# Optimization experiments

Hardware: AMD Instinct MI355X
Metric: run time of the kernel (lower is better)

## Reference

```python
import jax, jax.numpy as jnp
import numpy as np

B, S, F_IN, F_OUT, K = 4, 4096, 64, 64, 32


def setup_inputs() -> dict:
    key = jax.random.key(0)
    k1, k2, k3 = jax.random.split(key, 3)
    X = jax.random.normal(k1, (B, S, F_IN), dtype=jnp.float32)
    M = jax.random.normal(k2, (B, S, K), dtype=jnp.float32)
    # xavier_uniform for weight: bound = sqrt(6/(fan_in+fan_out))
    bound = float(np.sqrt(6.0 / (F_IN + F_OUT)))
    weight = jax.random.uniform(k3, (F_IN, F_OUT), dtype=jnp.float32,
                                minval=-bound, maxval=bound)
    bias = jnp.zeros((F_OUT,), dtype=jnp.float32)
    return {"X": X, "M": M, "weight": weight, "bias": bias}


def reference(X, M, weight, bias):
    # similarity = softmax(relu(M M^T), axis=-1)  -> [B, S, S]
    sim_raw = jnp.einsum('bsk,btk->bst', M, M)
    sim = jax.nn.softmax(jax.nn.relu(sim_raw), axis=-1)
    # X W  -> [B, S, F_OUT]
    Xw = jnp.einsum('bsf,fo->bso', X, weight)
    # mode='add': (I + A) Xw = Xw + A @ Xw  (identity matmul folded)
    Z = Xw + jnp.einsum('bst,bto->bso', sim, Xw)
    Z = Z + bias
    # dropout is identity at inference (eval mode)
    return Z
```

## Files before the change

### kernel.cpp

```cpp
#include <hip/hip_runtime.h>
#include <cstdint>

#define BATCH  4
#define SLEN   4096
#define FDIM   64
#define KDIM   32
#define KSPLIT 8
#define CHUNK  (SLEN / KSPLIT)

typedef __attribute__((ext_vector_type(8))) short bf16x8;
typedef __attribute__((ext_vector_type(4))) short bf16x4;
typedef __attribute__((ext_vector_type(4))) float f32x4;

static __device__ __forceinline__ short f2bf(float f) {
    union { float f; unsigned u; } v; v.f = f;
    unsigned r = v.u + 0x7fffu + ((v.u >> 16) & 1u);
    return (short)(r >> 16);
}
static __device__ __forceinline__ float bf2f(short s) {
    union { unsigned u; float f; } v;
    v.u = ((unsigned)(unsigned short)s) << 16;
    return v.f;
}
static __device__ __forceinline__ unsigned pack2bf(float a, float b) {
    union { float f; unsigned u; } x, y; x.f = a; y.f = b;
    unsigned ra = x.u + 0x7fffu + ((x.u >> 16) & 1u);
    unsigned rb = y.u + 0x7fffu + ((y.u >> 16) & 1u);
    return __builtin_amdgcn_perm(rb, ra, 0x07060302u);
}

__global__ __launch_bounds__(256) void prep(const float4* __restrict__ M4,
                                            ushort4* __restrict__ H4,
                                            ushort4* __restrict__ L4,
                                            const float* __restrict__ X,
                                            const float4* __restrict__ W4,
                                            float4* __restrict__ V4,
                                            short* __restrict__ Vt) {
    const int blk = blockIdx.y * gridDim.x + blockIdx.x;
#pragma unroll
    for (int r = 0; r < 2; ++r) {
        int i = (blk * 2 + r) * 256 + threadIdx.x;
        float4 m = M4[i];
        ushort4 h, l;
        h.x = (unsigned short)f2bf(m.x); l.x = (unsigned short)f2bf(m.x - bf2f((short)h.x));
        h.y = (unsigned short)f2bf(m.y); l.y = (unsigned short)f2bf(m.y - bf2f((short)h.y));
        h.z = (unsigned short)f2bf(m.z); l.z = (unsigned short)f2bf(m.z - bf2f((short)h.z));
        h.w = (unsigned short)f2bf(m.w); l.w = (unsigned short)f2bf(m.w - bf2f((short)h.w));
        H4[i] = h; L4[i] = l;
    }
    __shared__ float t[64][65];
    const int b  = blockIdx.y;
    const int s0 = blockIdx.x * 64;
    const int o4 = threadIdx.x & 15;
    const int rq = threadIdx.x >> 4;
#pragma unroll
    for (int half = 0; half < 4; ++half) {
        int r = half * 16 + rq;
        const float* __restrict__ xr = X + ((size_t)b * SLEN + s0 + r) * FDIM;
        float4 acc = make_float4(0.f, 0.f, 0.f, 0.f);
#pragma unroll
        for (int f = 0; f < FDIM; ++f) {
            float4 w = W4[f * 16 + o4];
            float  x = xr[f];
            acc.x = fmaf(x, w.x, acc.x);
            acc.y = fmaf(x, w.y, acc.y);
            acc.z = fmaf(x, w.z, acc.z);
            acc.w = fmaf(x, w.w, acc.w);
        }
        V4[((size_t)b * SLEN + s0 + r) * 16 + o4] = acc;
        t[r][o4 * 4 + 0] = acc.x;
        t[r][o4 * 4 + 1] = acc.y;
        t[r][o4 * 4 + 2] = acc.z;
        t[r][o4 * 4 + 3] = acc.w;
    }
    __syncthreads();
    const int c0 = threadIdx.x & 63;
    const int r0 = threadIdx.x >> 6;
#pragma unroll
    for (int i = 0; i < 16; ++i) {
        int f = r0 + i * 4;
        Vt[((size_t)b * FDIM + f) * SLEN + s0 + c0] = f2bf(t[c0][f]);
    }
}

__global__ __launch_bounds__(256, 3) void attn_mfma(const short* __restrict__ Mhi,
                                                    const short* __restrict__ Mlo,
                                                    const short* __restrict__ Vt,
                                                    float* __restrict__ accP,
                                                    float* __restrict__ lP) {
    const int bid  = blockIdx.x;
    const int slab = (bid & 7) + 8 * (bid >> 8);
    const int qblk = (bid >> 3) & 31;
    const int b    = slab >> 3;
    const int ks   = slab & 7;

    const int tid  = threadIdx.x;
    const int wave = tid >> 6;
    const int lane = tid & 63;
    const int col  = lane & 15;
    const int quad = lane >> 4;
    const int qbase = qblk * 128 + wave * 32;
    const int k0    = ks * CHUNK;

    const short* __restrict__ Mbh = Mhi + (size_t)b * SLEN * KDIM;
    const short* __restrict__ Mbl = Mlo + (size_t)b * SLEN * KDIM;
    const short* __restrict__ Vb  = Vt  + (size_t)b * FDIM * SLEN;

    __shared__ short khi[32 * 40];
    __shared__ short klo[32 * 40];
    __shared__ short vsh[64 * 40];

    bf16x8 Qh[2], Ql[2];
#pragma unroll
    for (int tq = 0; tq < 2; ++tq) {
        int qo = (qbase + tq * 16 + col) * KDIM + quad * 8;
        Qh[tq] = *(const bf16x8*)(Mbh + qo);
        Ql[tq] = *(const bf16x8*)(Mbl + qo);
    }

    f32x4 accf[2][4];
#pragma unroll
    for (int tq = 0; tq < 2; ++tq)
#pragma unroll
        for (int fg = 0; fg < 4; ++fg) accf[tq][fg] = (f32x4){0.f, 0.f, 0.f, 0.f};
    float lacc[2] = {0.f, 0.f};

    const int krow  = (tid & 127) >> 2;
    const int kpart = tid & 3;
    const int vrow  = tid >> 2;
    const short* __restrict__ Msrc = (tid < 128) ? Mbh : Mbl;
    short* __restrict__ kdst = (tid < 128) ? khi : klo;

#pragma unroll 1
    for (int kt = k0; kt < k0 + CHUNK; kt += 32) {
        bf16x8 kstg = *(const bf16x8*)(Msrc + (kt + krow) * KDIM + kpart * 8);
        bf16x8 vstg = *(const bf16x8*)(Vb + (size_t)vrow * SLEN + kt + kpart * 8);
        __syncthreads();
        *(bf16x8*)(kdst + krow * 40 + kpart * 8) = kstg;
        *(bf16x8*)(vsh + vrow * 40 + kpart * 8)  = vstg;
        __syncthreads();

        bf16x8 Kh0 = *(const bf16x8*)(khi + col * 40 + quad * 8);
        bf16x8 Kh1 = *(const bf16x8*)(khi + (16 + col) * 40 + quad * 8);
        bf16x8 Kl0 = *(const bf16x8*)(klo + col * 40 + quad * 8);
        bf16x8 Kl1 = *(const bf16x8*)(klo + (16 + col) * 40 + quad * 8);

        bf16x8 Vv[4];
#pragma unroll
        for (int fg = 0; fg < 4; ++fg) {
            const short* vp = vsh + (fg * 16 + col) * 40 + quad * 4;
            bf16x4 vlo = *(const bf16x4*)(vp);
            bf16x4 vhi = *(const bf16x4*)(vp + 16);
            Vv[fg] = __builtin_shufflevector(vlo, vhi, 0, 1, 2, 3, 4, 5, 6, 7);
        }

#pragma unroll
        for (int tq = 0; tq < 2; ++tq) {
            f32x4 z = (f32x4){0.f, 0.f, 0.f, 0.f};
            f32x4 c0 = __builtin_amdgcn_mfma_f32_16x16x32_bf16(Kh0, Ql[tq], z, 0, 0, 0);
            f32x4 c1 = __builtin_amdgcn_mfma_f32_16x16x32_bf16(Kh1, Ql[tq], z, 0, 0, 0);
            c0 = __builtin_amdgcn_mfma_f32_16x16x32_bf16(Kl0, Qh[tq], c0, 0, 0, 0);
            c1 = __builtin_amdgcn_mfma_f32_16x16x32_bf16(Kl1, Qh[tq], c1, 0, 0, 0);
            c0 = __builtin_amdgcn_mfma_f32_16x16x32_bf16(Kh0, Qh[tq], c0, 0, 0, 0);
            c1 = __builtin_amdgcn_mfma_f32_16x16x32_bf16(Kh1, Qh[tq], c1, 0, 0, 0);

            float e00 = __expf(fmaxf(c0[0], 0.f));
            float e01 = __expf(fmaxf(c0[1], 0.f));
            float e02 = __expf(fmaxf(c0[2], 0.f));
            float e03 = __expf(fmaxf(c0[3], 0.f));
            float e10 = __expf(fmaxf(c1[0], 0.f));
            float e11 = __expf(fmaxf(c1[1], 0.f));
            float e12 = __expf(fmaxf(c1[2], 0.f));
            float e13 = __expf(fmaxf(c1[3], 0.f));
            lacc[tq] += ((e00 + e01) + (e02 + e03)) + ((e10 + e11) + (e12 + e13));

            union { unsigned u[4]; bf16x8 v; } pa;
            pa.u[0] = pack2bf(e00, e01);
            pa.u[1] = pack2bf(e02, e03);
            pa.u[2] = pack2bf(e10, e11);
            pa.u[3] = pack2bf(e12, e13);

#pragma unroll
            for (int fg = 0; fg < 4; ++fg)
                accf[tq][fg] = __builtin_amdgcn_mfma_f32_16x16x32_bf16(
                    pa.v, Vv[fg], accf[tq][fg], 0, 0, 0);
        }
    }

#pragma unroll
    for (int tq = 0; tq < 2; ++tq) {
#pragma unroll
        for (int j = 0; j < 4; ++j) {
            int q = qbase + tq * 16 + quad * 4 + j;
            size_t base = ((size_t)b * SLEN + q) * KSPLIT + ks;
            float* __restrict__ op = accP + base * FDIM;
#pragma unroll
            for (int fg = 0; fg < 4; ++fg)
                op[fg * 16 + col] = accf[tq][fg][j];
        }
        float lv = lacc[tq];
        lv += __shfl_xor(lv, 16);
        lv += __shfl_xor(lv, 32);
        if (quad == 0) {
            int q = qbase + tq * 16 + col;
            lP[((size_t)b * SLEN + q) * KSPLIT + ks] = lv;
        }
    }
}

__global__ __launch_bounds__(256) void combine_kernel(const float4* __restrict__ V4,
                                                      const float4* __restrict__ accP4,
                                                      const float* __restrict__ lP,
                                                      const float4* __restrict__ bias4,
                                                      float4* __restrict__ out4) {
    int i  = blockIdx.x * 256 + threadIdx.x;
    int o4 = i & 15;
    int row = i >> 4;
    float nx = 0.f, ny = 0.f, nz = 0.f, nw = 0.f, den = 0.f;
#pragma unroll
    for (int k = 0; k < KSPLIT; ++k) {
        float4 a = accP4[((size_t)row * KSPLIT + k) * 16 + o4];
        nx += a.x; ny += a.y; nz += a.z; nw += a.w;
        den += lP[(size_t)row * KSPLIT + k];
    }
    float r = 1.f / den;
    float4 v = V4[i];
    float4 bb = bias4[o4];
    float4 o;
    o.x = v.x + nx * r + bb.x;
    o.y = v.y + ny * r + bb.y;
    o.z = v.z + nz * r + bb.z;
    o.w = v.w + nw * r + bb.w;
    out4[i] = o;
}

extern "C" void kernel_launch(void* const* d_in, const int* in_sizes, int n_in,
                              void* d_out, int out_size, void* d_ws, size_t ws_size,
                              hipStream_t stream) {
    const float* X    = (const float*)d_in[0];
    const float* M    = (const float*)d_in[1];
    const float* W    = (const float*)d_in[2];
    const float* bias = (const float*)d_in[3];
    float* out = (float*)d_out;

    const size_t vElems = (size_t)BATCH * SLEN * FDIM;
    const size_t mElems = (size_t)BATCH * SLEN * KDIM;
    const size_t rows   = (size_t)BATCH * SLEN;

    float* Vf   = (float*)d_ws;
    float* accP = Vf + vElems;
    float* lP   = accP + vElems * KSPLIT;
    short* Mhi  = (short*)(lP + rows * KSPLIT);
    short* Mlo  = Mhi + mElems;
    short* Vt   = Mlo + mElems;

    prep<<<dim3(SLEN / 64, BATCH), 256, 0, stream>>>(
        (const float4*)M, (ushort4*)Mhi, (ushort4*)Mlo,
        X, (const float4*)W, (float4*)Vf, Vt);

    attn_mfma<<<dim3((SLEN / 128) * BATCH * KSPLIT), 256, 0, stream>>>(
        Mhi, Mlo, Vt, accP, lP);

    combine_kernel<<<(int)(vElems / 1024), 256, 0, stream>>>(
        (const float4*)Vf, (const float4*)accP, lP, (const float4*)bias,
        (float4*)out);
}
```

Before: 120.7 us.

## Double-buffer LDS tiles in attention loop and switch to exp2 with prescaled M

The attention kernel now keeps two LDS buffers for the K and V tiles. It prefetches the next tile's global loads into registers while the current one is computed, which cuts the two barriers per iteration down to one and hides global load latency. M is prescaled by sqrt(log2 e) in prep, so the hardware exp2 replaces __expf without changing the math. It also raises wave priority around the MFMA section, gives prep more, smaller blocks with vectorized X loads, and vectorizes the denominator loads in combine. The cost is extra LDS use, which may limit occupancy, and a small rounding change from scaling before the bf16 split.

Measured after the change: 113.1 us. 6.4% less time.

```diff
diff --git a/kernel.cpp b/kernel.cpp
--- a/kernel.cpp
+++ b/kernel.cpp
@@ -7,10 +7,19 @@
 #define KDIM   32
 #define KSPLIT 8
 #define CHUNK  (SLEN / KSPLIT)
+#define NSTEP  (CHUNK / 32)
+
+#define MSCALE 1.2011224087864498f
 
 typedef __attribute__((ext_vector_type(8))) short bf16x8;
 typedef __attribute__((ext_vector_type(4))) short bf16x4;
 typedef __attribute__((ext_vector_type(4))) float f32x4;
+
+#if __has_builtin(__builtin_amdgcn_exp2f)
+#define EXP2(x) __builtin_amdgcn_exp2f(x)
+#else
+#define EXP2(x) exp2f(x)
+#endif
 
 static __device__ __forceinline__ short f2bf(float f) {
     union { float f; unsigned u; } v; v.f = f;
@@ -32,54 +41,55 @@
 __global__ __launch_bounds__(256) void prep(const float4* __restrict__ M4,
                                             ushort4* __restrict__ H4,
                                             ushort4* __restrict__ L4,
-                                            const float* __restrict__ X,
+                                            const float4* __restrict__ X4,
                                             const float4* __restrict__ W4,
                                             float4* __restrict__ V4,
                                             short* __restrict__ Vt) {
+    const int tid = threadIdx.x;
     const int blk = blockIdx.y * gridDim.x + blockIdx.x;
-#pragma unroll
-    for (int r = 0; r < 2; ++r) {
-        int i = (blk * 2 + r) * 256 + threadIdx.x;
+    if (blk < (BATCH * SLEN * KDIM) / (4 * 256)) {
+        int i = blk * 256 + tid;
         float4 m = M4[i];
+        float mx = m.x * MSCALE, my = m.y * MSCALE;
+        float mz = m.z * MSCALE, mw = m.w * MSCALE;
         ushort4 h, l;
-        h.x = (unsigned short)f2bf(m.x); l.x = (unsigned short)f2bf(m.x - bf2f((short)h.x));
-        h.y = (unsigned short)f2bf(m.y); l.y = (unsigned short)f2bf(m.y - bf2f((short)h.y));
-        h.z = (unsigned short)f2bf(m.z); l.z = (unsigned short)f2bf(m.z - bf2f((short)h.z));
-        h.w = (unsigned short)f2bf(m.w); l.w = (unsigned short)f2bf(m.w - bf2f((short)h.w));
+        h.x = (unsigned short)f2bf(mx); l.x = (unsigned short)f2bf(mx - bf2f((short)h.x));
+        h.y = (unsigned short)f2bf(my); l.y = (unsigned short)f2bf(my - bf2f((short)h.y));
+        h.z = (unsigned short)f2bf(mz); l.z = (unsigned short)f2bf(mz - bf2f((short)h.z));
+        h.w = (unsigned short)f2bf(mw); l.w = (unsigned short)f2bf(mw - bf2f((short)h.w));
         H4[i] = h; L4[i] = l;
     }
-    __shared__ float t[64][65];
+    __shared__ float t[16][68];
     const int b  = blockIdx.y;
-    const int s0 = blockIdx.x * 64;
-    const int o4 = threadIdx.x & 15;
-    const int rq = threadIdx.x >> 4;
-#pragma unroll
-    for (int half = 0; half < 4; ++half) {
-        int r = half * 16 + rq;
-        const float* __restrict__ xr = X + ((size_t)b * SLEN + s0 + r) * FDIM;
-        float4 acc = make_float4(0.f, 0.f, 0.f, 0.f);
-#pragma unroll
-        for (int f = 0; f < FDIM; ++f) {
-            float4 w = W4[f * 16 + o4];
-            float  x = xr[f];
-            acc.x = fmaf(x, w.x, acc.x);
-            acc.y = fmaf(x, w.y, acc.y);
-            acc.z = fmaf(x, w.z, acc.z);
-            acc.w = fmaf(x, w.w, acc.w);
-        }
-        V4[((size_t)b * SLEN + s0 + r) * 16 + o4] = acc;
-        t[r][o4 * 4 + 0] = acc.x;
-        t[r][o4 * 4 + 1] = acc.y;
-        t[r][o4 * 4 + 2] = acc.z;
-        t[r][o4 * 4 + 3] = acc.w;
-    }
+    const int s0 = blockIdx.x * 16;
+    const int r  = tid >> 4;
+    const int o4 = tid & 15;
+    const float4* __restrict__ xr = X4 + ((size_t)b * SLEN + s0 + r) * (FDIM / 4);
+    float4 acc = make_float4(0.f, 0.f, 0.f, 0.f);
+#pragma unroll
+    for (int f4 = 0; f4 < FDIM / 4; ++f4) {
+        float4 x  = xr[f4];
+        float4 w0 = W4[(f4 * 4 + 0) * 16 + o4];
+        float4 w1 = W4[(f4 * 4 + 1) * 16 + o4];
+        float4 w2 = W4[(f4 * 4 + 2) * 16 + o4];
+        float4 w3 = W4[(f4 * 4 + 3) * 16 + o4];
+        acc.x = fmaf(x.x, w0.x, fmaf(x.y, w1.x, fmaf(x.z, w2.x, fmaf(x.w, w3.x, acc.x))));
+        acc.y = fmaf(x.x, w0.y, fmaf(x.y, w1.y, fmaf(x.z, w2.y, fmaf(x.w, w3.y, acc.y))));
+        acc.z = fmaf(x.x, w0.z, fmaf(x.y, w1.z, fmaf(x.z, w2.z, fmaf(x.w, w3.z, acc.z))));
+        acc.w = fmaf(x.x, w0.w, fmaf(x.y, w1.w, fmaf(x.z, w2.w, fmaf(x.w, w3.w, acc.w))));
+    }
+    V4[((size_t)b * SLEN + s0 + r) * 16 + o4] = acc;
+    t[r][o4 * 4 + 0] = acc.x;
+    t[r][o4 * 4 + 1] = acc.y;
+    t[r][o4 * 4 + 2] = acc.z;
+    t[r][o4 * 4 + 3] = acc.w;
     __syncthreads();
-    const int c0 = threadIdx.x & 63;
-    const int r0 = threadIdx.x >> 6;
-#pragma unroll
-    for (int i = 0; i < 16; ++i) {
-        int f = r0 + i * 4;
-        Vt[((size_t)b * FDIM + f) * SLEN + s0 + c0] = f2bf(t[c0][f]);
+    const int c  = tid & 15;
+    const int f0 = tid >> 4;
+#pragma unroll
+    for (int i2 = 0; i2 < 4; ++i2) {
+        int f = f0 + i2 * 16;
+        Vt[((size_t)b * FDIM + f) * SLEN + s0 + c] = f2bf(t[c][f]);
     }
 }
 
@@ -106,9 +116,9 @@
     const short* __restrict__ Mbl = Mlo + (size_t)b * SLEN * KDIM;
     const short* __restrict__ Vb  = Vt  + (size_t)b * FDIM * SLEN;
 
-    __shared__ short khi[32 * 40];
-    __shared__ short klo[32 * 40];
-    __shared__ short vsh[64 * 40];
+    __shared__ short khi[2][32 * 40];
+    __shared__ short klo[2][32 * 40];
+    __shared__ short vsh[2][64 * 40];
 
     bf16x8 Qh[2], Ql[2];
 #pragma unroll
@@ -129,31 +139,47 @@
     const int kpart = tid & 3;
     const int vrow  = tid >> 2;
     const short* __restrict__ Msrc = (tid < 128) ? Mbh : Mbl;
-    short* __restrict__ kdst = (tid < 128) ? khi : klo;
+    const int koff  = krow * 40 + kpart * 8;
+    const int voff  = vrow * 40 + kpart * 8;
+    const int kgoff = krow * KDIM + kpart * 8;
+
+    bf16x8 kstg = *(const bf16x8*)(Msrc + (size_t)k0 * KDIM + kgoff);
+    bf16x8 vstg = *(const bf16x8*)(Vb + (size_t)vrow * SLEN + k0 + kpart * 8);
 
 #pragma unroll 1
-    for (int kt = k0; kt < k0 + CHUNK; kt += 32) {
-        bf16x8 kstg = *(const bf16x8*)(Msrc + (kt + krow) * KDIM + kpart * 8);
-        bf16x8 vstg = *(const bf16x8*)(Vb + (size_t)vrow * SLEN + kt + kpart * 8);
-        __syncthreads();
-        *(bf16x8*)(kdst + krow * 40 + kpart * 8) = kstg;
-        *(bf16x8*)(vsh + vrow * 40 + kpart * 8)  = vstg;
-        __syncthreads();
-
-        bf16x8 Kh0 = *(const bf16x8*)(khi + col * 40 + quad * 8);
-        bf16x8 Kh1 = *(const bf16x8*)(khi + (16 + col) * 40 + quad * 8);
-        bf16x8 Kl0 = *(const bf16x8*)(klo + col * 40 + quad * 8);
-        bf16x8 Kl1 = *(const bf16x8*)(klo + (16 + col) * 40 + quad * 8);
+    for (int step = 0; step < NSTEP; ++step) {
+        const int cur = step & 1;
+        short* __restrict__ kdst = (tid < 128) ? khi[cur] : klo[cur];
+        *(bf16x8*)(kdst + koff)     = kstg;
+        *(bf16x8*)(vsh[cur] + voff) = vstg;
+        if (step + 1 < NSTEP) {
+            int kt = k0 + (step + 1) * 32;
+            kstg = *(const bf16x8*)(Msrc + (size_t)kt * KDIM + kgoff);
+            vstg = *(const bf16x8*)(Vb + (size_t)vrow * SLEN + kt + kpart * 8);
+        }
+        asm volatile("s_waitcnt lgkmcnt(0)" ::: "memory");
+        __builtin_amdgcn_s_barrier();
+        __builtin_amdgcn_sched_barrier(0);
+
+        const short* __restrict__ kh = khi[cur];
+        const short* __restrict__ kl = klo[cur];
+        const short* __restrict__ vv = vsh[cur];
+
+        bf16x8 Kh0 = *(const bf16x8*)(kh + col * 40 + quad * 8);
+        bf16x8 Kh1 = *(const bf16x8*)(kh + (16 + col) * 40 + quad * 8);
+        bf16x8 Kl0 = *(const bf16x8*)(kl + col * 40 + quad * 8);
+        bf16x8 Kl1 = *(const bf16x8*)(kl + (16 + col) * 40 + quad * 8);
 
         bf16x8 Vv[4];
 #pragma unroll
         for (int fg = 0; fg < 4; ++fg) {
-            const short* vp = vsh + (fg * 16 + col) * 40 + quad * 4;
+            const short* vp = vv + (fg * 16 + col) * 40 + quad * 4;
             bf16x4 vlo = *(const bf16x4*)(vp);
             bf16x4 vhi = *(const bf16x4*)(vp + 16);
             Vv[fg] = __builtin_shufflevector(vlo, vhi, 0, 1, 2, 3, 4, 5, 6, 7);
         }
 
+        __builtin_amdgcn_s_setprio(1);
 #pragma unroll
         for (int tq = 0; tq < 2; ++tq) {
             f32x4 z = (f32x4){0.f, 0.f, 0.f, 0.f};
@@ -164,14 +190,14 @@
             c0 = __builtin_amdgcn_mfma_f32_16x16x32_bf16(Kh0, Qh[tq], c0, 0, 0, 0);
             c1 = __builtin_amdgcn_mfma_f32_16x16x32_bf16(Kh1, Qh[tq], c1, 0, 0, 0);
 
-            float e00 = __expf(fmaxf(c0[0], 0.f));
-            float e01 = __expf(fmaxf(c0[1], 0.f));
-            float e02 = __expf(fmaxf(c0[2], 0.f));
-            float e03 = __expf(fmaxf(c0[3], 0.f));
-            float e10 = __expf(fmaxf(c1[0], 0.f));
-            float e11 = __expf(fmaxf(c1[1], 0.f));
-            float e12 = __expf(fmaxf(c1[2], 0.f));
-            float e13 = __expf(fmaxf(c1[3], 0.f));
+            float e00 = EXP2(fmaxf(c0[0], 0.f));
+            float e01 = EXP2(fmaxf(c0[1], 0.f));
+            float e02 = EXP2(fmaxf(c0[2], 0.f));
+            float e03 = EXP2(fmaxf(c0[3], 0.f));
+            float e10 = EXP2(fmaxf(c1[0], 0.f));
+            float e11 = EXP2(fmaxf(c1[1], 0.f));
+            float e12 = EXP2(fmaxf(c1[2], 0.f));
+            float e13 = EXP2(fmaxf(c1[3], 0.f));
             lacc[tq] += ((e00 + e01) + (e02 + e03)) + ((e10 + e11) + (e12 + e13));
 
             union { unsigned u[4]; bf16x8 v; } pa;
@@ -185,6 +211,7 @@
                 accf[tq][fg] = __builtin_amdgcn_mfma_f32_16x16x32_bf16(
                     pa.v, Vv[fg], accf[tq][fg], 0, 0, 0);
         }
+        __builtin_amdgcn_s_setprio(0);
     }
 
 #pragma unroll
@@ -210,19 +237,21 @@
 
 __global__ __launch_bounds__(256) void combine_kernel(const float4* __restrict__ V4,
                                                       const float4* __restrict__ accP4,
-                                                      const float* __restrict__ lP,
+                                                      const float4* __restrict__ lP4,
                                                       const float4* __restrict__ bias4,
                                                       float4* __restrict__ out4) {
     int i  = blockIdx.x * 256 + threadIdx.x;
     int o4 = i & 15;
     int row = i >> 4;
-    float nx = 0.f, ny = 0.f, nz = 0.f, nw = 0.f, den = 0.f;
+    float nx = 0.f, ny = 0.f, nz = 0.f, nw = 0.f;
 #pragma unroll
     for (int k = 0; k < KSPLIT; ++k) {
         float4 a = accP4[((size_t)row * KSPLIT + k) * 16 + o4];
         nx += a.x; ny += a.y; nz += a.z; nw += a.w;
-        den += lP[(size_t)row * KSPLIT + k];
-    }
+    }
+    float4 l0 = lP4[(size_t)row * 2 + 0];
+    float4 l1 = lP4[(size_t)row * 2 + 1];
+    float den = ((l0.x + l0.y) + (l0.z + l0.w)) + ((l1.x + l1.y) + (l1.z + l1.w));
     float r = 1.f / den;
     float4 v = V4[i];
     float4 bb = bias4[o4];
@@ -254,14 +283,14 @@
     short* Mlo  = Mhi + mElems;
     short* Vt   = Mlo + mElems;
 
-    prep<<<dim3(SLEN / 64, BATCH), 256, 0, stream>>>(
+    prep<<<dim3(SLEN / 16, BATCH), 256, 0, stream>>>(
         (const float4*)M, (ushort4*)Mhi, (ushort4*)Mlo,
-        X, (const float4*)W, (float4*)Vf, Vt);
+        (const float4*)X, (const float4*)W, (float4*)Vf, Vt);
 
     attn_mfma<<<dim3((SLEN / 128) * BATCH * KSPLIT), 256, 0, stream>>>(
         Mhi, Mlo, Vt, accP, lP);
 
     combine_kernel<<<(int)(vElems / 1024), 256, 0, stream>>>(
-        (const float4*)Vf, (const float4*)accP, lP, (const float4*)bias,
-        (float4*)out);
-}
+        (const float4*)Vf, (const float4*)accP, (const float4*)lP,
+        (const float4*)bias, (float4*)out);
+}
```
